# Optimization experiments

Hardware: AMD Instinct MI355X
Metric: run time of the kernel (lower is better)

The kernel has to match this reference:

```python
import jax, jax.numpy as jnp
import numpy as np

H, W = 250, 400
N_RAYS = H * W          # 100000 (one patch)
N_SAMPLES = 1_000_000
P, C, DIM = 50000, 16, 8
STEP_SIZE = 0.005
DENSITY_SHIFT = 0.0
DENSITY_SCALE = min(1.0 / (1.0 - DENSITY_SHIFT), 25.0)


def setup_inputs() -> dict:
    key = jax.random.key(0)
    ks = jax.random.split(key, 12)
    return {
        "trivecs": jax.random.normal(ks[0], (P, C, 3, DIM), dtype=jnp.float32),
        "densities": jax.random.normal(ks[1], (P, C), dtype=jnp.float32),
        "colors": jax.random.normal(ks[2], (P, C, 3), dtype=jnp.float32),
        "local_gweight_s": jax.random.uniform(ks[3], (N_SAMPLES, 3), dtype=jnp.float32),
        "local_gweight_l": jax.random.uniform(ks[4], (N_SAMPLES, 3), dtype=jnp.float32),
        "t_min": jax.random.uniform(ks[5], (N_RAYS,), dtype=jnp.float32),
        "bg": jax.random.uniform(ks[6], (3,), dtype=jnp.float32),
        "local_gindx_s": jax.random.randint(ks[7], (N_SAMPLES, 3), 0, DIM, dtype=jnp.int32),
        "local_gindx_l": jax.random.randint(ks[8], (N_SAMPLES, 3), 0, DIM, dtype=jnp.int32),
        "tensoRF_id": jax.random.randint(ks[9], (N_SAMPLES,), 0, P, dtype=jnp.int32),
        "ray_id": jnp.sort(jax.random.randint(ks[10], (N_SAMPLES,), 0, N_RAYS, dtype=jnp.int32)),
        "step_id": jax.random.randint(ks[11], (N_SAMPLES,), 0, 200, dtype=jnp.int32),
    }


def reference(trivecs, densities, colors, local_gweight_s, local_gweight_l,
              t_min, bg, local_gindx_s, local_gindx_l, tensoRF_id, ray_id, step_id):
    # --- compute_feature: trilinear tensor-decomposition gather ---
    def interp(a):
        vs = trivecs[tensoRF_id, :, a, local_gindx_s[:, a]]  # [N, C]
        vl = trivecs[tensoRF_id, :, a, local_gindx_l[:, a]]  # [N, C]
        return vs * local_gweight_s[:, a:a + 1] + vl * local_gweight_l[:, a:a + 1]

    feature = interp(0) * interp(1) * interp(2)               # [N, C]
    sigma = (feature * densities[tensoRF_id]).sum(axis=1)     # [N]
    color = jnp.einsum('nc,nck->nk', feature, colors[tensoRF_id])  # [N, 3]

    # --- density activation & alpha ---
    density = jax.nn.softplus(sigma - DENSITY_SHIFT * 10.0) * DENSITY_SCALE
    alpha = 1.0 - jnp.exp(-density * STEP_SIZE)               # [N]

    # --- Alphas2Weights: per-ray exclusive transmittance (ray_id sorted) ---
    log_t = -density * STEP_SIZE                              # == log(1 - alpha)
    seg_total = jax.ops.segment_sum(log_t, ray_id, num_segments=N_RAYS)  # [R]
    seg_offset = jnp.concatenate([jnp.zeros((1,), log_t.dtype),
                                  jnp.cumsum(seg_total)[:-1]])           # [R]
    excl = jnp.cumsum(log_t) - log_t - seg_offset[ray_id]     # within-segment excl cumsum
    weights = alpha * jnp.exp(excl)                           # [N]
    bg_weight = jnp.exp(seg_total)                            # [R], prod(1-alpha) per ray

    # --- ray compositing ---
    rgb = jax.nn.sigmoid(color)                               # [N, 3]
    rgb_map = jax.ops.segment_sum(weights[:, None] * rgb, ray_id, num_segments=N_RAYS)
    rgb_map = rgb_map + bg_weight[:, None] * bg[None, :]
    z_val = t_min[ray_id] + step_id.astype(jnp.float32) * STEP_SIZE
    depth_map = jax.ops.segment_sum(weights * z_val, ray_id, num_segments=N_RAYS)
    alpha_map = 1.0 - bg_weight

    rgb_map = rgb_map.T.reshape(3, H, W)
    depth_map = depth_map.reshape(H, W)
    alpha_map = alpha_map.reshape(H, W)
    return rgb_map, depth_map, alpha_map
```

## Files before the change

kernel.cpp:

```cpp
#include <hip/hip_runtime.h>
#include <math.h>

#define HN       250
#define WN       400
#define N_RAYS   (HN * WN)
#define N_SAMP   1000000
#define P_TENSO  50000
#define C_CH     16
#define DIMV     8
#define STEP_SZ  0.005f
#define DENS_SCALE 1.0f

#define OFF_SDATA   0
#define OFF_RESULTS 32000000
#define OFF_COUNTS  48000000
#define OFF_STARTS  48200000
#define OFF_CURSOR  48400000
#define OFF_BSUMS   48600000
#define OFF_RSTART  48601024
#define WS_NEED     (48601024 + 400004 + 64)

__global__ __launch_bounds__(256) void zero_ints(int* p, int n) {
    int i = blockIdx.x * 256 + threadIdx.x;
    if (i < n) p[i] = 0;
}

__global__ __launch_bounds__(256) void hist_and_bounds(
    const int* __restrict__ tenso_id, const int* __restrict__ ray_id,
    int* __restrict__ counts, int* __restrict__ ray_start) {
    int n = blockIdx.x * 256 + threadIdx.x;
    if (n >= N_SAMP) return;
    atomicAdd(&counts[tenso_id[n]], 1);
    int r = ray_id[n];
    int rprev = (n == 0) ? -1 : ray_id[n - 1];
    for (int q = rprev + 1; q <= r; ++q) ray_start[q] = n;
    if (n == N_SAMP - 1) {
        for (int q = r + 1; q <= N_RAYS; ++q) ray_start[q] = N_SAMP;
    }
}

__global__ __launch_bounds__(256) void scan_local(const int* __restrict__ in,
                                                  int* __restrict__ out,
                                                  int* __restrict__ bsums, int n) {
    __shared__ int lds[256];
    const int t = threadIdx.x;
    const int base = blockIdx.x * 1024;
    int v[4]; int s = 0;
    #pragma unroll
    for (int i = 0; i < 4; ++i) {
        int idx = base + t * 4 + i;
        v[i] = (idx < n) ? in[idx] : 0;
        s += v[i];
    }
    lds[t] = s;
    __syncthreads();
    for (int d = 1; d < 256; d <<= 1) {
        int x = (t >= d) ? lds[t - d] : 0;
        __syncthreads();
        lds[t] += x;
        __syncthreads();
    }
    int run = (t > 0) ? lds[t - 1] : 0;
    #pragma unroll
    for (int i = 0; i < 4; ++i) {
        int idx = base + t * 4 + i;
        if (idx < n) out[idx] = run;
        run += v[i];
    }
    if (t == 255) bsums[blockIdx.x] = lds[255];
}

__global__ __launch_bounds__(64) void scan_totals(int* __restrict__ bsums, int nb) {
    int t = threadIdx.x;
    int v = (t < nb) ? bsums[t] : 0;
    #pragma unroll
    for (int d = 1; d < 64; d <<= 1) {
        int u = __shfl_up(v, d, 64);
        if (t >= d) v += u;
    }
    int excl = __shfl_up(v, 1, 64);
    if (t == 0) excl = 0;
    if (t < nb) bsums[t] = excl;
}

__global__ __launch_bounds__(256) void scan_add(int* __restrict__ starts,
                                                int* __restrict__ cursor,
                                                const int* __restrict__ bsums, int n) {
    int i = blockIdx.x * 256 + threadIdx.x;
    if (i < n) { int v = starts[i] + bsums[i >> 10]; starts[i] = v; cursor[i] = v; }
}

__global__ __launch_bounds__(256) void scatter_samples(
    const int*   __restrict__ tenso_id,
    const int*   __restrict__ gis, const int* __restrict__ gil,
    const float* __restrict__ gws, const float* __restrict__ gwl,
    int* __restrict__ cursor,
    float4* __restrict__ sdata)
{
    int n = blockIdx.x * 256 + threadIdx.x;
    if (n >= N_SAMP) return;
    int tid = tenso_id[n];
    int pos = atomicAdd(&cursor[tid], 1);
    unsigned bits = (unsigned)gis[n*3+0] | ((unsigned)gis[n*3+1] << 3) | ((unsigned)gis[n*3+2] << 6)
                  | ((unsigned)gil[n*3+0] << 9) | ((unsigned)gil[n*3+1] << 12) | ((unsigned)gil[n*3+2] << 15);
    float4 A = make_float4(gws[n*3+0], gws[n*3+1], gws[n*3+2], gwl[n*3+0]);
    float4 B = make_float4(gwl[n*3+1], gwl[n*3+2], __uint_as_float(bits), __uint_as_float((unsigned)n));
    sdata[(size_t)pos * 2 + 0] = A;
    sdata[(size_t)pos * 2 + 1] = B;
}

#define ROW_STRIDE 20
#define TV_F   (24 * ROW_STRIDE)
#define SLAB_F (TV_F + 16 + 48)
__global__ __launch_bounds__(256) void gather_phase(
    const float* __restrict__ trivecs,
    const float* __restrict__ densities,
    const float* __restrict__ colors,
    const int*   __restrict__ starts,
    const int*   __restrict__ counts,
    const float4* __restrict__ sdata,
    float* __restrict__ results_f)
{
    __shared__ __align__(16) float lds[4 * SLAB_F];
    const int lane = threadIdx.x & 63;
    const int wv   = threadIdx.x >> 6;
    const int t    = blockIdx.x * 4 + wv;
    if (t >= P_TENSO) return;

    const int start = starts[t];
    const int cnt   = counts[t];
    if (cnt == 0) return;

    float* slab = lds + wv * SLAB_F;
    float* dl   = slab + TV_F;
    float* cl   = dl + 16;

    const float* tvg = trivecs + (size_t)t * 384;
    #pragma unroll
    for (int i = 0; i < 6; ++i) {
        int l = lane + i * 64;
        int c = l / 24;
        int rem = l - c * 24;
        slab[rem * ROW_STRIDE + c] = tvg[l];
    }
    if (lane < 16) dl[lane] = densities[(size_t)t * 16 + lane];
    if (lane < 48) {
        int c = lane / 3, k = lane - c * 3;
        cl[k * 16 + c] = colors[(size_t)t * 48 + lane];
    }

    const int g = lane >> 2;
    const int j = lane & 3;

    const float4 dens4 = *(const float4*)(dl + 4 * j);
    const float4 col0  = *(const float4*)(cl + 4 * j);
    const float4 col1  = *(const float4*)(cl + 16 + 4 * j);
    const float4 col2  = *(const float4*)(cl + 32 + 4 * j);

    const int end = start + cnt;
    const int niter = (cnt + 15) >> 4;

    for (int it = 0; it < niter; ++it) {
        const int pos = start + it * 16 + g;
        const bool valid = (pos < end);
        const int cp = valid ? pos : (end - 1);
        const float4 A = sdata[(size_t)cp * 2 + 0];
        const float4 B = sdata[(size_t)cp * 2 + 1];
        const unsigned bits = __float_as_uint(B.z);
        const unsigned orig = __float_as_uint(B.w);

        float4 f;
        {
            const int is = bits & 7, il = (bits >> 9) & 7;
            const float4 vs = *(const float4*)(slab + is * ROW_STRIDE + 4 * j);
            const float4 vl = *(const float4*)(slab + il * ROW_STRIDE + 4 * j);
            f.x = vs.x * A.x + vl.x * A.w;
            f.y = vs.y * A.x + vl.y * A.w;
            f.z = vs.z * A.x + vl.z * A.w;
            f.w = vs.w * A.x + vl.w * A.w;
        }
        {
            const int is = (bits >> 3) & 7, il = (bits >> 12) & 7;
            const float4 vs = *(const float4*)(slab + 8 * ROW_STRIDE + is * ROW_STRIDE + 4 * j);
            const float4 vl = *(const float4*)(slab + 8 * ROW_STRIDE + il * ROW_STRIDE + 4 * j);
            f.x *= vs.x * A.y + vl.x * B.x;
            f.y *= vs.y * A.y + vl.y * B.x;
            f.z *= vs.z * A.y + vl.z * B.x;
            f.w *= vs.w * A.y + vl.w * B.x;
        }
        {
            const int is = (bits >> 6) & 7, il = (bits >> 15) & 7;
            const float4 vs = *(const float4*)(slab + 16 * ROW_STRIDE + is * ROW_STRIDE + 4 * j);
            const float4 vl = *(const float4*)(slab + 16 * ROW_STRIDE + il * ROW_STRIDE + 4 * j);
            f.x *= vs.x * A.z + vl.x * B.y;
            f.y *= vs.y * A.z + vl.y * B.y;
            f.z *= vs.z * A.z + vl.z * B.y;
            f.w *= vs.w * A.z + vl.w * B.y;
        }

        float s0 = f.x * dens4.x + f.y * dens4.y + f.z * dens4.z + f.w * dens4.w;
        float s1 = f.x * col0.x  + f.y * col0.y  + f.z * col0.z  + f.w * col0.w;
        float s2 = f.x * col1.x  + f.y * col1.y  + f.z * col1.z  + f.w * col1.w;
        float s3 = f.x * col2.x  + f.y * col2.y  + f.z * col2.z  + f.w * col2.w;

        s0 += __shfl_xor(s0, 1); s0 += __shfl_xor(s0, 2);
        s1 += __shfl_xor(s1, 1); s1 += __shfl_xor(s1, 2);
        s2 += __shfl_xor(s2, 1); s2 += __shfl_xor(s2, 2);
        s3 += __shfl_xor(s3, 1); s3 += __shfl_xor(s3, 2);

        const float sj = (j == 0) ? s0 : (j == 1) ? s1 : (j == 2) ? s2 : s3;
        float val;
        if (j == 0) {
            float dens = fmaxf(sj, 0.0f) + __logf(1.0f + __expf(-fabsf(sj)));
            val = -(dens * DENS_SCALE) * STEP_SZ;
        } else {
            val = 1.0f / (1.0f + __expf(-sj));
        }
        if (valid) results_f[(size_t)orig * 4 + j] = val;
    }
}

__global__ __launch_bounds__(256) void ray_render(
    const float4* __restrict__ results,
    const float*  __restrict__ t_min,
    const float*  __restrict__ bg,
    const int*    __restrict__ ray_start,
    const int*    __restrict__ step_id,
    float* __restrict__ out)
{
    int r = blockIdx.x * 256 + threadIdx.x;
    if (r >= N_RAYS) return;
    const int s = ray_start[r];
    const int e = ray_start[r + 1];
    const float tmin_r = t_min[r];

    float T = 0.0f, aR = 0.0f, aG = 0.0f, aB = 0.0f, aD = 0.0f;
    for (int n = s; n < e; ++n) {
        float4 res = results[n];
        const float lt = res.x;
        const float w = (1.0f - __expf(lt)) * __expf(T);
        T += lt;
        const float z = tmin_r + (float)step_id[n] * STEP_SZ;
        aR += w * res.y;
        aG += w * res.z;
        aB += w * res.w;
        aD += w * z;
    }
    const float bgw = __expf(T);
    out[0 * N_RAYS + r] = aR + bgw * bg[0];
    out[1 * N_RAYS + r] = aG + bgw * bg[1];
    out[2 * N_RAYS + r] = aB + bgw * bg[2];
    out[3 * N_RAYS + r] = aD;
    out[4 * N_RAYS + r] = 1.0f - bgw;
}

__global__ __launch_bounds__(256) void trivec_render_fallback(
    const float* __restrict__ trivecs, const float* __restrict__ densities,
    const float* __restrict__ colors, const float* __restrict__ gws,
    const float* __restrict__ gwl, const float* __restrict__ t_min,
    const float* __restrict__ bg, const int* __restrict__ gis,
    const int* __restrict__ gil, const int* __restrict__ tenso_id,
    const int* __restrict__ ray_id, const int* __restrict__ step_id,
    float* __restrict__ out)
{
    const int lane = threadIdx.x & 63;
    const int r = blockIdx.x * 4 + (threadIdx.x >> 6);
    if (r >= N_RAYS) return;
    const int c = lane & 15;
    const int g = lane >> 4;
    int lo = 0, hi = N_SAMP;
    while (lo < hi) { int mid = (lo + hi) >> 1; if (ray_id[mid] < r) lo = mid + 1; else hi = mid; }
    const int seg_start = lo;
    hi = N_SAMP;
    while (lo < hi) { int mid = (lo + hi) >> 1; if (ray_id[mid] < r + 1) lo = mid + 1; else hi = mid; }
    const int seg_end = lo;
    const float tmin_r = t_min[r];
    float Tlog = 0.0f, accR = 0.0f, accG = 0.0f, accB = 0.0f, accD = 0.0f;
    const int niter = (seg_end - seg_start + 3) >> 2;
    for (int it = 0; it < niter; ++it) {
        const int n = seg_start + it * 4 + g;
        const bool valid = (n < seg_end);
        const int nc = valid ? n : (seg_end - 1);
        const int tid = tenso_id[nc];
        const float* tv = trivecs + (size_t)tid * 384 + c * 24;
        float f = 1.0f;
        #pragma unroll
        for (int a = 0; a < 3; ++a) {
            const int is = gis[nc*3+a], il = gil[nc*3+a];
            const float wS = gws[nc*3+a], wL = gwl[nc*3+a];
            f *= (tv[a*8+is] * wS + tv[a*8+il] * wL);
        }
        const float dns = densities[(size_t)tid * 16 + c];
        const float* colp = colors + ((size_t)tid * 16 + c) * 3;
        float s0 = f*dns, s1 = f*colp[0], s2 = f*colp[1], s3 = f*colp[2];
        #pragma unroll
        for (int m = 1; m < 16; m <<= 1) {
            s0 += __shfl_xor(s0, m); s1 += __shfl_xor(s1, m);
            s2 += __shfl_xor(s2, m); s3 += __shfl_xor(s3, m);
        }
        float dens = fmaxf(s0, 0.0f) + __logf(1.0f + __expf(-fabsf(s0)));
        const float lt = valid ? (-dens * STEP_SZ) : 0.0f;
        const float alpha = 1.0f - __expf(lt);
        const float rr = 1.0f/(1.0f+__expf(-s1)), gg = 1.0f/(1.0f+__expf(-s2)), bb = 1.0f/(1.0f+__expf(-s3));
        const float z = tmin_r + (float)step_id[nc] * STEP_SZ;
        const float lt0 = __shfl(lt,0), lt1 = __shfl(lt,16), lt2 = __shfl(lt,32), lt3 = __shfl(lt,48);
        float excl = Tlog;
        if (g > 0) excl += lt0;
        if (g > 1) excl += lt1;
        if (g > 2) excl += lt2;
        const float w = alpha * __expf(excl);
        Tlog += lt0 + lt1 + lt2 + lt3;
        accR += w*rr; accG += w*gg; accB += w*bb; accD += w*z;
    }
    accR += __shfl_xor(accR,16); accR += __shfl_xor(accR,32);
    accG += __shfl_xor(accG,16); accG += __shfl_xor(accG,32);
    accB += __shfl_xor(accB,16); accB += __shfl_xor(accB,32);
    accD += __shfl_xor(accD,16); accD += __shfl_xor(accD,32);
    const float bgw = __expf(Tlog);
    if (lane == 0) {
        out[0*N_RAYS+r] = accR + bgw*bg[0];
        out[1*N_RAYS+r] = accG + bgw*bg[1];
        out[2*N_RAYS+r] = accB + bgw*bg[2];
        out[3*N_RAYS+r] = accD;
        out[4*N_RAYS+r] = 1.0f - bgw;
    }
}

extern "C" void kernel_launch(void* const* d_in, const int* in_sizes, int n_in,
                              void* d_out, int out_size, void* d_ws, size_t ws_size,
                              hipStream_t stream) {
    const float* trivecs   = (const float*)d_in[0];
    const float* densities = (const float*)d_in[1];
    const float* colors    = (const float*)d_in[2];
    const float* gws       = (const float*)d_in[3];
    const float* gwl       = (const float*)d_in[4];
    const float* t_min     = (const float*)d_in[5];
    const float* bg        = (const float*)d_in[6];
    const int*   gis       = (const int*)d_in[7];
    const int*   gil       = (const int*)d_in[8];
    const int*   tenso_id  = (const int*)d_in[9];
    const int*   ray_id    = (const int*)d_in[10];
    const int*   step_id   = (const int*)d_in[11];
    float* out = (float*)d_out;

    if (ws_size < (size_t)WS_NEED) {
        trivec_render_fallback<<<(N_RAYS + 3) / 4, 256, 0, stream>>>(
            trivecs, densities, colors, gws, gwl, t_min, bg,
            gis, gil, tenso_id, ray_id, step_id, out);
        return;
    }

    char* ws = (char*)d_ws;
    float4* sdata    = (float4*)(ws + OFF_SDATA);
    float4* results  = (float4*)(ws + OFF_RESULTS);
    int*    counts   = (int*)(ws + OFF_COUNTS);
    int*    starts   = (int*)(ws + OFF_STARTS);
    int*    cursor   = (int*)(ws + OFF_CURSOR);
    int*    bsums    = (int*)(ws + OFF_BSUMS);
    int*    raystart = (int*)(ws + OFF_RSTART);

    const int NB = (P_TENSO + 1023) / 1024;

    zero_ints<<<(P_TENSO + 255) / 256, 256, 0, stream>>>(counts, P_TENSO);
    hist_and_bounds<<<(N_SAMP + 255) / 256, 256, 0, stream>>>(tenso_id, ray_id, counts, raystart);
    scan_local<<<NB, 256, 0, stream>>>(counts, starts, bsums, P_TENSO);
    scan_totals<<<1, 64, 0, stream>>>(bsums, NB);
    scan_add<<<(P_TENSO + 255) / 256, 256, 0, stream>>>(starts, cursor, bsums, P_TENSO);
    scatter_samples<<<(N_SAMP + 255) / 256, 256, 0, stream>>>(
        tenso_id, gis, gil, gws, gwl, cursor, sdata);
    gather_phase<<<(P_TENSO + 3) / 4, 256, 0, stream>>>(
        trivecs, densities, colors, starts, counts, sdata, (float*)results);
    ray_render<<<(N_RAYS + 255) / 256, 256, 0, stream>>>(
        results, t_min, bg, raystart, step_id, out);
}
```

Baseline: 313.7 us.

## Fuse all pipeline stages into one cooperative persistent kernel with grid syncs

Replaces the eight separate kernel launches (zero, histogram, three scan stages, scatter, gather, ray render) with a single cooperative persistent kernel. Each stage uses grid-stride loops, and grid.sync() separates the stages. The goal is to remove per-launch overhead and inter-kernel gaps. The cost is that grid-wide barriers replace launch boundaries, and the grid is capped at 1024 blocks, which may lower parallelism for the gather and scatter phases. The original multi-kernel path is kept as a fallback if the cooperative launch fails.

```diff
diff --git a/kernel.cpp b/kernel.cpp
--- a/kernel.cpp
+++ b/kernel.cpp
@@ -1,15 +1,17 @@
 #include <hip/hip_runtime.h>
+#include <hip/hip_cooperative_groups.h>
 #include <math.h>
+
+namespace cg = cooperative_groups;
 
 #define HN       250
 #define WN       400
 #define N_RAYS   (HN * WN)
 #define N_SAMP   1000000
 #define P_TENSO  50000
-#define C_CH     16
-#define DIMV     8
 #define STEP_SZ  0.005f
 #define DENS_SCALE 1.0f
+#define NB_SCAN  ((P_TENSO + 1023) / 1024)
 
 #define OFF_SDATA   0
 #define OFF_RESULTS 32000000
@@ -19,6 +21,247 @@
 #define OFF_BSUMS   48600000
 #define OFF_RSTART  48601024
 #define WS_NEED     (48601024 + 400004 + 64)
+
+#define ROW_STRIDE 20
+#define TV_F   (24 * ROW_STRIDE)
+#define SLAB_F (TV_F + 16 + 48)
+
+#define MEGA_BLOCKS_MAX 1024
+
+__global__ __launch_bounds__(256, 4) void mega_kernel(
+    const float* __restrict__ trivecs,
+    const float* __restrict__ densities,
+    const float* __restrict__ colors,
+    const float* __restrict__ gws,
+    const float* __restrict__ gwl,
+    const float* __restrict__ t_min,
+    const float* __restrict__ bg,
+    const int*   __restrict__ gis,
+    const int*   __restrict__ gil,
+    const int*   __restrict__ tenso_id,
+    const int*   __restrict__ ray_id,
+    const int*   __restrict__ step_id,
+    float* __restrict__ out,
+    float4* __restrict__ sdata,
+    float4* __restrict__ results,
+    int* __restrict__ counts,
+    int* __restrict__ starts,
+    int* __restrict__ cursor,
+    int* __restrict__ bsums,
+    int* __restrict__ ray_start)
+{
+    cg::grid_group grid = cg::this_grid();
+    const int tix = blockIdx.x * 256 + threadIdx.x;
+    const int gsz = gridDim.x * 256;
+    __shared__ __align__(16) float smem[4 * SLAB_F];
+
+    for (int i = tix; i < P_TENSO; i += gsz) counts[i] = 0;
+    grid.sync();
+
+    for (int n = tix; n < N_SAMP; n += gsz) {
+        atomicAdd(&counts[tenso_id[n]], 1);
+        int r = ray_id[n];
+        int rprev = (n == 0) ? -1 : ray_id[n - 1];
+        for (int q = rprev + 1; q <= r; ++q) ray_start[q] = n;
+        if (n == N_SAMP - 1) {
+            for (int q = r + 1; q <= N_RAYS; ++q) ray_start[q] = N_SAMP;
+        }
+    }
+    grid.sync();
+
+    {
+        int* ilds = (int*)smem;
+        const int b = blockIdx.x;
+        if (b < NB_SCAN) {
+            const int t = threadIdx.x;
+            const int base = b * 1024;
+            int v[4]; int s = 0;
+            #pragma unroll
+            for (int i = 0; i < 4; ++i) {
+                int idx = base + t * 4 + i;
+                v[i] = (idx < P_TENSO) ? counts[idx] : 0;
+                s += v[i];
+            }
+            ilds[t] = s;
+            __syncthreads();
+            for (int d = 1; d < 256; d <<= 1) {
+                int x = (t >= d) ? ilds[t - d] : 0;
+                __syncthreads();
+                ilds[t] += x;
+                __syncthreads();
+            }
+            int run = (t > 0) ? ilds[t - 1] : 0;
+            #pragma unroll
+            for (int i = 0; i < 4; ++i) {
+                int idx = base + t * 4 + i;
+                if (idx < P_TENSO) starts[idx] = run;
+                run += v[i];
+            }
+            if (t == 255) bsums[b] = ilds[255];
+        }
+    }
+    grid.sync();
+
+    {
+        int* bscan = (int*)smem;
+        if (threadIdx.x < 64) {
+            int t = threadIdx.x;
+            int v = (t < NB_SCAN) ? bsums[t] : 0;
+            int incl = v;
+            #pragma unroll
+            for (int d = 1; d < 64; d <<= 1) {
+                int u = __shfl_up(incl, d, 64);
+                if (t >= d) incl += u;
+            }
+            if (t < NB_SCAN) bscan[t] = incl - v;
+        }
+        __syncthreads();
+        for (int i = tix; i < P_TENSO; i += gsz) {
+            int v = starts[i] + bscan[i >> 10];
+            starts[i] = v;
+            cursor[i] = v;
+        }
+    }
+    grid.sync();
+
+    for (int n = tix; n < N_SAMP; n += gsz) {
+        int tid = tenso_id[n];
+        int pos = atomicAdd(&cursor[tid], 1);
+        unsigned bits = (unsigned)gis[n*3+0] | ((unsigned)gis[n*3+1] << 3) | ((unsigned)gis[n*3+2] << 6)
+                      | ((unsigned)gil[n*3+0] << 9) | ((unsigned)gil[n*3+1] << 12) | ((unsigned)gil[n*3+2] << 15);
+        float4 A = make_float4(gws[n*3+0], gws[n*3+1], gws[n*3+2], gwl[n*3+0]);
+        float4 B = make_float4(gwl[n*3+1], gwl[n*3+2], __uint_as_float(bits), __uint_as_float((unsigned)n));
+        sdata[(size_t)pos * 2 + 0] = A;
+        sdata[(size_t)pos * 2 + 1] = B;
+    }
+    grid.sync();
+
+    {
+        float* results_f = (float*)results;
+        const int lane = threadIdx.x & 63;
+        const int wv   = threadIdx.x >> 6;
+        const int gwave  = blockIdx.x * 4 + wv;
+        const int nwaves = gridDim.x * 4;
+        float* slab = smem + wv * SLAB_F;
+        float* dl   = slab + TV_F;
+        float* cl   = dl + 16;
+        const int g = lane >> 2;
+        const int j = lane & 3;
+
+        for (int t = gwave; t < P_TENSO; t += nwaves) {
+            const int start = starts[t];
+            const int cnt   = counts[t];
+            if (cnt == 0) continue;
+
+            const float* tvg = trivecs + (size_t)t * 384;
+            #pragma unroll
+            for (int i = 0; i < 6; ++i) {
+                int l = lane + i * 64;
+                int c = l / 24;
+                int rem = l - c * 24;
+                slab[rem * ROW_STRIDE + c] = tvg[l];
+            }
+            if (lane < 16) dl[lane] = densities[(size_t)t * 16 + lane];
+            if (lane < 48) {
+                int c = lane / 3, k = lane - c * 3;
+                cl[k * 16 + c] = colors[(size_t)t * 48 + lane];
+            }
+
+            const float4 dens4 = *(const float4*)(dl + 4 * j);
+            const float4 col0  = *(const float4*)(cl + 4 * j);
+            const float4 col1  = *(const float4*)(cl + 16 + 4 * j);
+            const float4 col2  = *(const float4*)(cl + 32 + 4 * j);
+
+            const int end = start + cnt;
+            const int niter = (cnt + 15) >> 4;
+
+            for (int it = 0; it < niter; ++it) {
+                const int pos = start + it * 16 + g;
+                const bool valid = (pos < end);
+                const int cp = valid ? pos : (end - 1);
+                const float4 A = sdata[(size_t)cp * 2 + 0];
+                const float4 B = sdata[(size_t)cp * 2 + 1];
+                const unsigned bits = __float_as_uint(B.z);
+                const unsigned orig = __float_as_uint(B.w);
+
+                float4 f;
+                {
+                    const int is = bits & 7, il = (bits >> 9) & 7;
+                    const float4 vs = *(const float4*)(slab + is * ROW_STRIDE + 4 * j);
+                    const float4 vl = *(const float4*)(slab + il * ROW_STRIDE + 4 * j);
+                    f.x = vs.x * A.x + vl.x * A.w;
+                    f.y = vs.y * A.x + vl.y * A.w;
+                    f.z = vs.z * A.x + vl.z * A.w;
+                    f.w = vs.w * A.x + vl.w * A.w;
+                }
+                {
+                    const int is = (bits >> 3) & 7, il = (bits >> 12) & 7;
+                    const float4 vs = *(const float4*)(slab + (8 + is) * ROW_STRIDE + 4 * j);
+                    const float4 vl = *(const float4*)(slab + (8 + il) * ROW_STRIDE + 4 * j);
+                    f.x *= vs.x * A.y + vl.x * B.x;
+                    f.y *= vs.y * A.y + vl.y * B.x;
+                    f.z *= vs.z * A.y + vl.z * B.x;
+                    f.w *= vs.w * A.y + vl.w * B.x;
+                }
+                {
+                    const int is = (bits >> 6) & 7, il = (bits >> 15) & 7;
+                    const float4 vs = *(const float4*)(slab + (16 + is) * ROW_STRIDE + 4 * j);
+                    const float4 vl = *(const float4*)(slab + (16 + il) * ROW_STRIDE + 4 * j);
+                    f.x *= vs.x * A.z + vl.x * B.y;
+                    f.y *= vs.y * A.z + vl.y * B.y;
+                    f.z *= vs.z * A.z + vl.z * B.y;
+                    f.w *= vs.w * A.z + vl.w * B.y;
+                }
+
+                float s0 = f.x * dens4.x + f.y * dens4.y + f.z * dens4.z + f.w * dens4.w;
+                float s1 = f.x * col0.x  + f.y * col0.y  + f.z * col0.z  + f.w * col0.w;
+                float s2 = f.x * col1.x  + f.y * col1.y  + f.z * col1.z  + f.w * col1.w;
+                float s3 = f.x * col2.x  + f.y * col2.y  + f.z * col2.z  + f.w * col2.w;
+
+                s0 += __shfl_xor(s0, 1); s0 += __shfl_xor(s0, 2);
+                s1 += __shfl_xor(s1, 1); s1 += __shfl_xor(s1, 2);
+                s2 += __shfl_xor(s2, 1); s2 += __shfl_xor(s2, 2);
+                s3 += __shfl_xor(s3, 1); s3 += __shfl_xor(s3, 2);
+
+                const float sj = (j == 0) ? s0 : (j == 1) ? s1 : (j == 2) ? s2 : s3;
+                float val;
+                if (j == 0) {
+                    float dens = fmaxf(sj, 0.0f) + __logf(1.0f + __expf(-fabsf(sj)));
+                    val = -(dens * DENS_SCALE) * STEP_SZ;
+                } else {
+                    val = 1.0f / (1.0f + __expf(-sj));
+                }
+                if (valid) results_f[(size_t)orig * 4 + j] = val;
+            }
+        }
+    }
+    grid.sync();
+
+    for (int r = tix; r < N_RAYS; r += gsz) {
+        const int s = ray_start[r];
+        const int e = ray_start[r + 1];
+        const float tmin_r = t_min[r];
+
+        float T = 0.0f, aR = 0.0f, aG = 0.0f, aB = 0.0f, aD = 0.0f;
+        for (int n = s; n < e; ++n) {
+            float4 res = results[n];
+            const float lt = res.x;
+            const float w = (1.0f - __expf(lt)) * __expf(T);
+            T += lt;
+            const float z = tmin_r + (float)step_id[n] * STEP_SZ;
+            aR += w * res.y;
+            aG += w * res.z;
+            aB += w * res.w;
+            aD += w * z;
+        }
+        const float bgw = __expf(T);
+        out[0 * N_RAYS + r] = aR + bgw * bg[0];
+        out[1 * N_RAYS + r] = aG + bgw * bg[1];
+        out[2 * N_RAYS + r] = aB + bgw * bg[2];
+        out[3 * N_RAYS + r] = aD;
+        out[4 * N_RAYS + r] = 1.0f - bgw;
+    }
+}
 
 __global__ __launch_bounds__(256) void zero_ints(int* p, int n) {
     int i = blockIdx.x * 256 + threadIdx.x;
@@ -109,9 +352,6 @@
     sdata[(size_t)pos * 2 + 1] = B;
 }
 
-#define ROW_STRIDE 20
-#define TV_F   (24 * ROW_STRIDE)
-#define SLAB_F (TV_F + 16 + 48)
 __global__ __launch_bounds__(256) void gather_phase(
     const float* __restrict__ trivecs,
     const float* __restrict__ densities,
@@ -181,8 +421,8 @@
         }
         {
             const int is = (bits >> 3) & 7, il = (bits >> 12) & 7;
-            const float4 vs = *(const float4*)(slab + 8 * ROW_STRIDE + is * ROW_STRIDE + 4 * j);
-            const float4 vl = *(const float4*)(slab + 8 * ROW_STRIDE + il * ROW_STRIDE + 4 * j);
+            const float4 vs = *(const float4*)(slab + (8 + is) * ROW_STRIDE + 4 * j);
+            const float4 vl = *(const float4*)(slab + (8 + il) * ROW_STRIDE + 4 * j);
             f.x *= vs.x * A.y + vl.x * B.x;
             f.y *= vs.y * A.y + vl.y * B.x;
             f.z *= vs.z * A.y + vl.z * B.x;
@@ -190,8 +430,8 @@
         }
         {
             const int is = (bits >> 6) & 7, il = (bits >> 15) & 7;
-            const float4 vs = *(const float4*)(slab + 16 * ROW_STRIDE + is * ROW_STRIDE + 4 * j);
-            const float4 vl = *(const float4*)(slab + 16 * ROW_STRIDE + il * ROW_STRIDE + 4 * j);
+            const float4 vs = *(const float4*)(slab + (16 + is) * ROW_STRIDE + 4 * j);
+            const float4 vl = *(const float4*)(slab + (16 + il) * ROW_STRIDE + 4 * j);
             f.x *= vs.x * A.z + vl.x * B.y;
             f.y *= vs.y * A.z + vl.y * B.y;
             f.z *= vs.z * A.z + vl.z * B.y;
@@ -359,8 +599,34 @@
     int*    bsums    = (int*)(ws + OFF_BSUMS);
     int*    raystart = (int*)(ws + OFF_RSTART);
 
-    const int NB = (P_TENSO + 1023) / 1024;
-
+    bool coop_ok = false;
+    {
+        int blocksPerCU = 0;
+        hipError_t e1 = hipOccupancyMaxActiveBlocksPerMultiprocessor(
+            &blocksPerCU, (const void*)mega_kernel, 256, 0);
+        int nCU = 0;
+        hipError_t e2 = hipDeviceGetAttribute(&nCU, hipDeviceAttributeMultiprocessorCount, 0);
+        if (e1 == hipSuccess && e2 == hipSuccess && blocksPerCU > 0 && nCU > 0) {
+            int blocks = blocksPerCU * nCU;
+            if (blocks > MEGA_BLOCKS_MAX) blocks = MEGA_BLOCKS_MAX;
+            if (blocks >= 64) {
+                void* args[] = {
+                    (void*)&trivecs, (void*)&densities, (void*)&colors,
+                    (void*)&gws, (void*)&gwl, (void*)&t_min, (void*)&bg,
+                    (void*)&gis, (void*)&gil, (void*)&tenso_id, (void*)&ray_id,
+                    (void*)&step_id, (void*)&out,
+                    (void*)&sdata, (void*)&results, (void*)&counts, (void*)&starts,
+                    (void*)&cursor, (void*)&bsums, (void*)&raystart
+                };
+                hipError_t e3 = hipLaunchCooperativeKernel(
+                    (void*)mega_kernel, dim3(blocks), dim3(256), args, 0, stream);
+                coop_ok = (e3 == hipSuccess);
+            }
+        }
+    }
+    if (coop_ok) return;
+
+    const int NB = NB_SCAN;
     zero_ints<<<(P_TENSO + 255) / 256, 256, 0, stream>>>(counts, P_TENSO);
     hist_and_bounds<<<(N_SAMP + 255) / 256, 256, 0, stream>>>(tenso_id, ray_id, counts, raystart);
     scan_local<<<NB, 256, 0, stream>>>(counts, starts, bsums, P_TENSO);
```

Measured after the change: 831.5 us. +165.1%, slower.

## Replace scattered sample payload with permutation indices and indirect reads

Applied to the files above, without the earlier changes.

Samples are packed in original order with coalesced writes, and the scatter pass now writes only a permutation and its inverse. The gather kernel reads packed data through the permutation and writes results in sorted-by-tensor order. The ray renderer reads results through the inverse permutation. This trades large random writes for random reads plus extra index arrays, and adds an indirection latency in the sequential per-ray loop.

```diff
diff --git a/kernel.cpp b/kernel.cpp
--- a/kernel.cpp
+++ b/kernel.cpp
@@ -6,31 +6,52 @@
 #define N_RAYS   (HN * WN)
 #define N_SAMP   1000000
 #define P_TENSO  50000
-#define C_CH     16
-#define DIMV     8
 #define STEP_SZ  0.005f
 #define DENS_SCALE 1.0f
-
-#define OFF_SDATA   0
+#define NB_SCAN  ((P_TENSO + 1023) / 1024)
+
+
+#define OFF_PACK    0
 #define OFF_RESULTS 32000000
-#define OFF_COUNTS  48000000
-#define OFF_STARTS  48200000
-#define OFF_CURSOR  48400000
-#define OFF_BSUMS   48600000
-#define OFF_RSTART  48601024
-#define WS_NEED     (48601024 + 400004 + 64)
+#define OFF_PERM    48000000
+#define OFF_IPERM   52000000
+#define OFF_COUNTS  56000000
+#define OFF_STARTS  56200000
+#define OFF_CURSOR  56400000
+#define OFF_BSUMS   56600000
+#define OFF_RSTART  56601024
+#define WS_NEED     (56601024 + 400004 + 64)
+
+#define ROW_STRIDE 20
+#define TV_F   (24 * ROW_STRIDE)
+#define SLAB_F (TV_F + 16 + 48)
 
 __global__ __launch_bounds__(256) void zero_ints(int* p, int n) {
     int i = blockIdx.x * 256 + threadIdx.x;
     if (i < n) p[i] = 0;
 }
 
-__global__ __launch_bounds__(256) void hist_and_bounds(
-    const int* __restrict__ tenso_id, const int* __restrict__ ray_id,
-    int* __restrict__ counts, int* __restrict__ ray_start) {
+__global__ __launch_bounds__(256) void pack_hist_bounds(
+    const int*   __restrict__ tenso_id,
+    const int*   __restrict__ ray_id,
+    const int*   __restrict__ gis, const int* __restrict__ gil,
+    const float* __restrict__ gws, const float* __restrict__ gwl,
+    int* __restrict__ counts,
+    int* __restrict__ ray_start,
+    float4* __restrict__ pack)
+{
     int n = blockIdx.x * 256 + threadIdx.x;
     if (n >= N_SAMP) return;
+
     atomicAdd(&counts[tenso_id[n]], 1);
+
+    unsigned bits = (unsigned)gis[n*3+0] | ((unsigned)gis[n*3+1] << 3) | ((unsigned)gis[n*3+2] << 6)
+                  | ((unsigned)gil[n*3+0] << 9) | ((unsigned)gil[n*3+1] << 12) | ((unsigned)gil[n*3+2] << 15);
+    float4 A = make_float4(gws[n*3+0], gws[n*3+1], gws[n*3+2], gwl[n*3+0]);
+    float4 B = make_float4(gwl[n*3+1], gwl[n*3+2], __uint_as_float(bits), 0.0f);
+    pack[(size_t)n * 2 + 0] = A;
+    pack[(size_t)n * 2 + 1] = B;
+
     int r = ray_id[n];
     int rprev = (n == 0) ? -1 : ray_id[n - 1];
     for (int q = rprev + 1; q <= r; ++q) ray_start[q] = n;
@@ -90,35 +111,28 @@
     if (i < n) { int v = starts[i] + bsums[i >> 10]; starts[i] = v; cursor[i] = v; }
 }
 
-__global__ __launch_bounds__(256) void scatter_samples(
-    const int*   __restrict__ tenso_id,
-    const int*   __restrict__ gis, const int* __restrict__ gil,
-    const float* __restrict__ gws, const float* __restrict__ gwl,
+__global__ __launch_bounds__(256) void scatter_perm(
+    const int* __restrict__ tenso_id,
     int* __restrict__ cursor,
-    float4* __restrict__ sdata)
+    int* __restrict__ perm,
+    int* __restrict__ iperm)
 {
     int n = blockIdx.x * 256 + threadIdx.x;
     if (n >= N_SAMP) return;
     int tid = tenso_id[n];
     int pos = atomicAdd(&cursor[tid], 1);
-    unsigned bits = (unsigned)gis[n*3+0] | ((unsigned)gis[n*3+1] << 3) | ((unsigned)gis[n*3+2] << 6)
-                  | ((unsigned)gil[n*3+0] << 9) | ((unsigned)gil[n*3+1] << 12) | ((unsigned)gil[n*3+2] << 15);
-    float4 A = make_float4(gws[n*3+0], gws[n*3+1], gws[n*3+2], gwl[n*3+0]);
-    float4 B = make_float4(gwl[n*3+1], gwl[n*3+2], __uint_as_float(bits), __uint_as_float((unsigned)n));
-    sdata[(size_t)pos * 2 + 0] = A;
-    sdata[(size_t)pos * 2 + 1] = B;
-}
-
-#define ROW_STRIDE 20
-#define TV_F   (24 * ROW_STRIDE)
-#define SLAB_F (TV_F + 16 + 48)
+    perm[pos] = n;
+    iperm[n] = pos;
+}
+
 __global__ __launch_bounds__(256) void gather_phase(
     const float* __restrict__ trivecs,
     const float* __restrict__ densities,
     const float* __restrict__ colors,
     const int*   __restrict__ starts,
     const int*   __restrict__ counts,
-    const float4* __restrict__ sdata,
+    const int*   __restrict__ perm,
+    const float4* __restrict__ pack,
     float* __restrict__ results_f)
 {
     __shared__ __align__(16) float lds[4 * SLAB_F];
@@ -164,10 +178,10 @@
         const int pos = start + it * 16 + g;
         const bool valid = (pos < end);
         const int cp = valid ? pos : (end - 1);
-        const float4 A = sdata[(size_t)cp * 2 + 0];
-        const float4 B = sdata[(size_t)cp * 2 + 1];
+        const int n = perm[cp];
+        const float4 A = pack[(size_t)n * 2 + 0];
+        const float4 B = pack[(size_t)n * 2 + 1];
         const unsigned bits = __float_as_uint(B.z);
-        const unsigned orig = __float_as_uint(B.w);
 
         float4 f;
         {
@@ -181,8 +195,8 @@
         }
         {
             const int is = (bits >> 3) & 7, il = (bits >> 12) & 7;
-            const float4 vs = *(const float4*)(slab + 8 * ROW_STRIDE + is * ROW_STRIDE + 4 * j);
-            const float4 vl = *(const float4*)(slab + 8 * ROW_STRIDE + il * ROW_STRIDE + 4 * j);
+            const float4 vs = *(const float4*)(slab + (8 + is) * ROW_STRIDE + 4 * j);
+            const float4 vl = *(const float4*)(slab + (8 + il) * ROW_STRIDE + 4 * j);
             f.x *= vs.x * A.y + vl.x * B.x;
             f.y *= vs.y * A.y + vl.y * B.x;
             f.z *= vs.z * A.y + vl.z * B.x;
@@ -190,8 +204,8 @@
         }
         {
             const int is = (bits >> 6) & 7, il = (bits >> 15) & 7;
-            const float4 vs = *(const float4*)(slab + 16 * ROW_STRIDE + is * ROW_STRIDE + 4 * j);
-            const float4 vl = *(const float4*)(slab + 16 * ROW_STRIDE + il * ROW_STRIDE + 4 * j);
+            const float4 vs = *(const float4*)(slab + (16 + is) * ROW_STRIDE + 4 * j);
+            const float4 vl = *(const float4*)(slab + (16 + il) * ROW_STRIDE + 4 * j);
             f.x *= vs.x * A.z + vl.x * B.y;
             f.y *= vs.y * A.z + vl.y * B.y;
             f.z *= vs.z * A.z + vl.z * B.y;
@@ -216,12 +230,13 @@
         } else {
             val = 1.0f / (1.0f + __expf(-sj));
         }
-        if (valid) results_f[(size_t)orig * 4 + j] = val;
+        if (valid) results_f[(size_t)pos * 4 + j] = val;
     }
 }
 
 __global__ __launch_bounds__(256) void ray_render(
     const float4* __restrict__ results,
+    const int*    __restrict__ iperm,
     const float*  __restrict__ t_min,
     const float*  __restrict__ bg,
     const int*    __restrict__ ray_start,
@@ -236,7 +251,8 @@
 
     float T = 0.0f, aR = 0.0f, aG = 0.0f, aB = 0.0f, aD = 0.0f;
     for (int n = s; n < e; ++n) {
-        float4 res = results[n];
+        const int pos = iperm[n];
+        float4 res = results[pos];
         const float lt = res.x;
         const float w = (1.0f - __expf(lt)) * __expf(T);
         T += lt;
@@ -351,25 +367,25 @@
     }
 
     char* ws = (char*)d_ws;
-    float4* sdata    = (float4*)(ws + OFF_SDATA);
+    float4* pack     = (float4*)(ws + OFF_PACK);
     float4* results  = (float4*)(ws + OFF_RESULTS);
+    int*    perm     = (int*)(ws + OFF_PERM);
+    int*    iperm    = (int*)(ws + OFF_IPERM);
     int*    counts   = (int*)(ws + OFF_COUNTS);
     int*    starts   = (int*)(ws + OFF_STARTS);
     int*    cursor   = (int*)(ws + OFF_CURSOR);
     int*    bsums    = (int*)(ws + OFF_BSUMS);
     int*    raystart = (int*)(ws + OFF_RSTART);
 
-    const int NB = (P_TENSO + 1023) / 1024;
-
     zero_ints<<<(P_TENSO + 255) / 256, 256, 0, stream>>>(counts, P_TENSO);
-    hist_and_bounds<<<(N_SAMP + 255) / 256, 256, 0, stream>>>(tenso_id, ray_id, counts, raystart);
-    scan_local<<<NB, 256, 0, stream>>>(counts, starts, bsums, P_TENSO);
-    scan_totals<<<1, 64, 0, stream>>>(bsums, NB);
+    pack_hist_bounds<<<(N_SAMP + 255) / 256, 256, 0, stream>>>(
+        tenso_id, ray_id, gis, gil, gws, gwl, counts, raystart, pack);
+    scan_local<<<NB_SCAN, 256, 0, stream>>>(counts, starts, bsums, P_TENSO);
+    scan_totals<<<1, 64, 0, stream>>>(bsums, NB_SCAN);
     scan_add<<<(P_TENSO + 255) / 256, 256, 0, stream>>>(starts, cursor, bsums, P_TENSO);
-    scatter_samples<<<(N_SAMP + 255) / 256, 256, 0, stream>>>(
-        tenso_id, gis, gil, gws, gwl, cursor, sdata);
+    scatter_perm<<<(N_SAMP + 255) / 256, 256, 0, stream>>>(tenso_id, cursor, perm, iperm);
     gather_phase<<<(P_TENSO + 3) / 4, 256, 0, stream>>>(
-        trivecs, densities, colors, starts, counts, sdata, (float*)results);
+        trivecs, densities, colors, starts, counts, perm, pack, (float*)results);
     ray_render<<<(N_RAYS + 255) / 256, 256, 0, stream>>>(
-        results, t_min, bg, raystart, step_id, out);
-}
+        results, iperm, t_min, bg, raystart, step_id, out);
+}
```

Result: slower. 336.0 us (+7.1%).
